# Kernel optimization log

Measured on AMD Instinct MI355X. Metric: run time of the kernel, lower is better.

Reference implementation:

```python
import jax, jax.numpy as jnp
import numpy as np

H = 16  # num_heads


def _sinusoidal_positions(n_pos, d, dtype=jnp.float32):
    half = d // 2
    freqs = 1.0 / 10000 ** (jnp.arange(0, half, dtype=dtype) / float(half))
    pos = jnp.arange(n_pos, dtype=dtype)[:, None]
    angles = pos * freqs[None, :]
    emb = jnp.concatenate([jnp.sin(angles), jnp.cos(angles)], axis=-1)
    if d % 2 == 1:
        emb = jnp.pad(emb, ((0, 0), (0, 1)))
    return emb.astype(dtype)


def setup_inputs() -> dict:
    key = jax.random.key(0)
    B, M, C = 64, 2048, 1024
    D = C // H
    ks = jax.random.split(key, 12)
    s = 1.0 / np.sqrt(C)
    return {
        "x": jax.random.normal(ks[0], (B, C), jnp.float32),
        "mem": jax.random.normal(ks[1], (B, M, C), jnp.float32),
        "Wq": jax.random.normal(ks[2], (C, C), jnp.float32) * s,
        "bq": jnp.zeros((C,), jnp.float32),
        "Wk": jax.random.normal(ks[3], (C, C), jnp.float32) * s,
        "bk": jnp.zeros((C,), jnp.float32),
        "Wv": jax.random.normal(ks[4], (C, C), jnp.float32) * s,
        "bv": jnp.zeros((C,), jnp.float32),
        "u_bias": jax.random.normal(ks[5], (H, D), jnp.float32) * 0.02,
        "v_bias": jax.random.normal(ks[6], (H, D), jnp.float32) * 0.02,
        "Wo": jax.random.normal(ks[7], (C, C), jnp.float32) * s,
        "bo": jnp.zeros((C,), jnp.float32),
    }


def reference(x, mem, Wq, bq, Wk, bk, Wv, bv, u_bias, v_bias, Wo, bo):
    B, C = x.shape
    D = C // H
    M = mem.shape[1]
    L = M + 1
    cat = jnp.concatenate([mem, x[:, None, :]], axis=1)  # (B, L, C)
    q = (x @ Wq + bq).reshape(B, H, D)
    k = (cat @ Wk + bk).reshape(B, L, H, D)
    v = (cat @ Wv + bv).reshape(B, L, H, D)
    r = _sinusoidal_positions(L, D)[::-1, :]  # (L, D), reversed
    scale = 1.0 / jnp.sqrt(jnp.float32(D))
    ac = jnp.einsum('bhd,blhd->bhl', q + u_bias[None, :, :], k)
    bd = jnp.einsum('bhd,ld->bhl', q + v_bias[None, :, :], r)
    attn = jax.nn.softmax((ac + bd) * scale, axis=-1)
    out = jnp.einsum('bhl,blhd->bhd', attn, v).reshape(B, C)
    return out @ Wo + bo
```

## Files before the change

### kernel.cpp

```cpp
#include <hip/hip_runtime.h>
#include <hip/hip_bf16.h>
#include <math.h>

#define B   64
#define C   1024
#define HH  16
#define DD  64
#define MM  2048
#define LL  2049
#define SCALE 0.125f
#define NCHC 9
#define CHC  228
#define LCH  16
#define LCHR 129

template <int CTRL>
__device__ __forceinline__ float dpp_add(float keep, float send) {
  int moved =
      __builtin_amdgcn_update_dpp(0, __float_as_int(send), CTRL, 0xF, 0xF, true);
  return keep + __int_as_float(moved);
}

__global__ __launch_bounds__(256) void k_gemm(
    const float* __restrict__ A, int a_row_stride, int a_bx_off,
    const float* __restrict__ W, float* __restrict__ P) {
  __shared__ __attribute__((aligned(16))) float a_s[64 * 132];
  __shared__ __attribute__((aligned(16))) float b_s[128 * 68];
  int t = threadIdx.x;
  int jt = blockIdx.x, kc = blockIdx.y;
  const float* Ab = A + (size_t)jt * a_bx_off;
  int k0 = kc * 128;
  for (int idx = t; idx < 2048; idx += 256) {
    int bb = idx >> 5, f4 = idx & 31;
    float4 v = *(const float4*)&Ab[(size_t)bb * a_row_stride + k0 + 4 * f4];
    *(float4*)&a_s[bb * 132 + 4 * f4] = v;
  }
  for (int idx = t; idx < 2048; idx += 256) {
    int kk = idx >> 4, f4 = idx & 15;
    float4 v = *(const float4*)&W[(size_t)(k0 + kk) * 1024 + jt * 64 + 4 * f4];
    *(float4*)&b_s[kk * 68 + 4 * f4] = v;
  }
  __syncthreads();
  int j0 = (t & 15) * 4, b0 = (t >> 4) * 4;
  float4 acc[4];
#pragma unroll
  for (int i = 0; i < 4; ++i) acc[i] = make_float4(0.f, 0.f, 0.f, 0.f);
  for (int k = 0; k < 128; k += 4) {
    float4 w0 = *(const float4*)&b_s[(k + 0) * 68 + j0];
    float4 w1 = *(const float4*)&b_s[(k + 1) * 68 + j0];
    float4 w2 = *(const float4*)&b_s[(k + 2) * 68 + j0];
    float4 w3 = *(const float4*)&b_s[(k + 3) * 68 + j0];
#pragma unroll
    for (int i = 0; i < 4; ++i) {
      float4 av = *(const float4*)&a_s[(b0 + i) * 132 + k];
      acc[i].x += av.x * w0.x + av.y * w1.x + av.z * w2.x + av.w * w3.x;
      acc[i].y += av.x * w0.y + av.y * w1.y + av.z * w2.y + av.w * w3.y;
      acc[i].z += av.x * w0.z + av.y * w1.z + av.z * w2.z + av.w * w3.z;
      acc[i].w += av.x * w0.w + av.y * w1.w + av.z * w2.w + av.w * w3.w;
    }
  }
  size_t ob = (size_t)kc * 65536 + jt * 64;
#pragma unroll
  for (int i = 0; i < 4; ++i)
    *(float4*)&P[ob + (size_t)(b0 + i) * 1024 + j0] = acc[i];
}

__global__ __launch_bounds__(256) void k_reduce_qp(
    const float* __restrict__ P, const float* __restrict__ bq,
    const float* __restrict__ u, const float* __restrict__ v,
    float* __restrict__ qu, float* __restrict__ qv) {
  int idx = blockIdx.x * 256 + threadIdx.x;
  int b = idx >> 8, f4 = idx & 255;
  size_t off = (size_t)b * 1024 + 4 * f4;
  float4 s = *(const float4*)&P[off];
#pragma unroll
  for (int kc = 1; kc < 8; ++kc) {
    float4 t4 = *(const float4*)&P[(size_t)kc * 65536 + off];
    s.x += t4.x; s.y += t4.y; s.z += t4.z; s.w += t4.w;
  }
  float4 bb = *(const float4*)&bq[4 * f4];
  s.x += bb.x; s.y += bb.y; s.z += bb.z; s.w += bb.w;
  float4 uu = *(const float4*)&u[4 * f4];
  float4 vv = *(const float4*)&v[4 * f4];
  float4 o1 = make_float4(s.x + uu.x, s.y + uu.y, s.z + uu.z, s.w + uu.w);
  float4 o2 = make_float4(s.x + vv.x, s.y + vv.y, s.z + vv.z, s.w + vv.w);
  *(float4*)&qu[off] = o1;
  *(float4*)&qv[off] = o2;
}

__global__ __launch_bounds__(256) void k_reduce1(
    const float* __restrict__ P, const float* __restrict__ bias,
    float* __restrict__ out) {
  int idx = blockIdx.x * 256 + threadIdx.x;
  int b = idx >> 8, f4 = idx & 255;
  size_t off = (size_t)b * 1024 + 4 * f4;
  float4 s = *(const float4*)&P[off];
#pragma unroll
  for (int kc = 1; kc < 8; ++kc) {
    float4 t4 = *(const float4*)&P[(size_t)kc * 65536 + off];
    s.x += t4.x; s.y += t4.y; s.z += t4.z; s.w += t4.w;
  }
  float4 bb = *(const float4*)&bias[4 * f4];
  s.x += bb.x; s.y += bb.y; s.z += bb.z; s.w += bb.w;
  *(float4*)&out[off] = s;
}

__global__ __launch_bounds__(256) void k_wtilde(
    const float* __restrict__ qu, const float* __restrict__ Wk,
    float* __restrict__ wt) {
  __shared__ __attribute__((aligned(16))) float a_s[64 * 68];
  __shared__ __attribute__((aligned(16))) float w_s[64 * 68];
  int t = threadIdx.x, ct = blockIdx.x, h = blockIdx.y;
  for (int idx = t; idx < 1024; idx += 256) {
    int bb = idx >> 4, f4 = idx & 15;
    *(float4*)&a_s[bb * 68 + 4 * f4] =
        *(const float4*)&qu[(size_t)bb * 1024 + h * 64 + 4 * f4];
  }
  for (int idx = t; idx < 1024; idx += 256) {
    int cc = idx >> 4, f4 = idx & 15;
    *(float4*)&w_s[cc * 68 + 4 * f4] =
        *(const float4*)&Wk[(size_t)(ct * 64 + cc) * 1024 + h * 64 + 4 * f4];
  }
  __syncthreads();
  int c0 = (t & 15) * 4, b0 = (t >> 4) * 4;
  float acc[4][4] = {};
  for (int d = 0; d < 64; d += 4) {
    float4 w0 = *(const float4*)&w_s[(c0 + 0) * 68 + d];
    float4 w1 = *(const float4*)&w_s[(c0 + 1) * 68 + d];
    float4 w2 = *(const float4*)&w_s[(c0 + 2) * 68 + d];
    float4 w3 = *(const float4*)&w_s[(c0 + 3) * 68 + d];
#pragma unroll
    for (int i = 0; i < 4; ++i) {
      float4 av = *(const float4*)&a_s[(b0 + i) * 68 + d];
      acc[i][0] += av.x * w0.x + av.y * w0.y + av.z * w0.z + av.w * w0.w;
      acc[i][1] += av.x * w1.x + av.y * w1.y + av.z * w1.z + av.w * w1.w;
      acc[i][2] += av.x * w2.x + av.y * w2.y + av.z * w2.z + av.w * w2.w;
      acc[i][3] += av.x * w3.x + av.y * w3.y + av.z * w3.z + av.w * w3.w;
    }
  }
#pragma unroll
  for (int i = 0; i < 4; ++i) {
    float4 o = make_float4(acc[i][0], acc[i][1], acc[i][2], acc[i][3]);
    *(float4*)&wt[(size_t)((b0 + i) * 16 + h) * 1024 + ct * 64 + c0] = o;
  }
}

__global__ void k_rtab(float* __restrict__ rtab) {
  int idx = blockIdx.x * 256 + threadIdx.x;
  if (idx >= LL * 64) return;
  int l = idx >> 6, d = idx & 63;
  float p = (float)(LL - 1 - l);
  int dd = d & 31;
  float f = 1.0f / powf(10000.0f, (float)dd * (1.0f / 32.0f));
  float a = p * f;
  rtab[idx] = (d < 32) ? sinf(a) : cosf(a);
}

__global__ __launch_bounds__(256) void k_bd(
    const float* __restrict__ qv, const float* __restrict__ rtab,
    float* __restrict__ bd) {
  __shared__ __attribute__((aligned(16))) float rt_s[128 * 68];
  int t = threadIdx.x, ch = blockIdx.x, b = blockIdx.y;
  int l0 = ch * 128;
  int nrows = min(128, LL - l0);
  for (int idx = t; idx < nrows * 16; idx += 256) {
    int r = idx >> 4, d4 = idx & 15;
    *(float4*)&rt_s[r * 68 + 4 * d4] =
        *(const float4*)&rtab[(size_t)(l0 + r) * 64 + 4 * d4];
  }
  __syncthreads();
  for (int idx = t; idx < 16 * 128; idx += 256) {
    int h = idx >> 7, r = idx & 127;
    if (r < nrows) {
      const float* qh = &qv[(size_t)b * 1024 + h * 64];
      const float* rr = &rt_s[r * 68];
      float s = 0.f;
#pragma unroll
      for (int d4 = 0; d4 < 16; ++d4) {
        float4 rv = *(const float4*)&rr[4 * d4];
        float4 qq = *(const float4*)&qh[4 * d4];
        s += rv.x * qq.x + rv.y * qq.y + rv.z * qq.z + rv.w * qq.w;
      }
      bd[(size_t)(b * 16 + h) * LL + l0 + r] = s;
    }
  }
}

__global__ __launch_bounds__(256, 4) void k_logits(
    const float* __restrict__ x, const float* __restrict__ mem,
    const float* __restrict__ wt, const float* __restrict__ bd,
    float* __restrict__ logits) {
  __shared__ float red_s[LCHR * 68];
  int t = threadIdx.x;
  int lane = t & 63, w = t >> 6;
  int b = blockIdx.y, ch = blockIdx.x;
  int l0 = ch * LCHR, lend = min(LL, l0 + LCHR);
  int c_off = w * 256 + lane * 4;
  float4 wr[16];
#pragma unroll
  for (int h = 0; h < 16; ++h)
    wr[h] = *(const float4*)&wt[(size_t)(b * 16 + h) * 1024 + c_off];
  const float* xrow = &x[(size_t)b * 1024 + c_off];
  const float* memb = &mem[(size_t)b * MM * 1024 + c_off];
  bool u0 = (lane & 1) != 0, u1 = (lane & 2) != 0;
  bool u2 = (lane & 4) != 0, u3 = (lane & 8) != 0;
  int hmap = ((lane & 1) << 3) | ((lane & 2) << 1) | ((lane & 4) >> 1) |
             ((lane & 8) >> 3);

#define LOADROWS(dst, base)                                                  \
  {                                                                          \
    _Pragma("unroll") for (int r = 0; r < 4; ++r) {                          \
      int l = min((base) + r, LL - 1);                                       \
      dst[r] = *(const float4*)((l < MM) ? &memb[(size_t)l * 1024] : xrow);  \
    }                                                                        \
  }
#define COMPROWS(src, base)                                                  \
  {                                                                          \
    _Pragma("unroll") for (int r = 0; r < 4; ++r) {                          \
      int row = (base) + r;                                                  \
      if (row < lend) {                                                      \
        float4 rv = src[r];                                                  \
        float p[16];                                                         \
        _Pragma("unroll") for (int h = 0; h < 16; ++h)                       \
            p[h] = rv.x * wr[h].x + rv.y * wr[h].y + rv.z * wr[h].z +        \
                   rv.w * wr[h].w;                                           \
        _Pragma("unroll") for (int i = 0; i < 8; ++i) {                      \
          float send = u0 ? p[i] : p[i + 8];                                 \
          float keep = u0 ? p[i + 8] : p[i];                                 \
          p[i] = dpp_add<0xB1>(keep, send);                                  \
        }                                                                    \
        _Pragma("unroll") for (int i = 0; i < 4; ++i) {                      \
          float send = u1 ? p[i] : p[i + 4];                                 \
          float keep = u1 ? p[i + 4] : p[i];                                 \
          p[i] = dpp_add<0x4E>(keep, send);                                  \
        }                                                                    \
        _Pragma("unroll") for (int i = 0; i < 2; ++i) {                      \
          float send = u2 ? p[i] : p[i + 2];                                 \
          float keep = u2 ? p[i + 2] : p[i];                                 \
          p[i] = keep + __shfl_xor(send, 4, 64);                             \
        }                                                                    \
        {                                                                    \
          float send = u3 ? p[0] : p[1];                                     \
          float keep = u3 ? p[1] : p[0];                                     \
          float u = dpp_add<0x128>(keep, send);                              \
          u += __shfl_xor(u, 16, 64);                                        \
          u += __shfl_xor(u, 32, 64);                                        \
          if (lane < 16) red_s[(row - l0) * 68 + w * 16 + hmap] = u;         \
        }                                                                    \
      }                                                                      \
    }                                                                        \
  }

  float4 rbA[4], rbB[4];
  LOADROWS(rbA, l0)
  for (int g0 = l0; g0 < lend; g0 += 8) {
    LOADROWS(rbB, g0 + 4)
    COMPROWS(rbA, g0)
    if (g0 + 8 < lend) LOADROWS(rbA, g0 + 8)
    COMPROWS(rbB, g0 + 4)
  }
#undef LOADROWS
#undef COMPROWS

  __syncthreads();
  int nrows = lend - l0;
  for (int idx = t; idx < 16 * LCHR; idx += 256) {
    int h = idx / LCHR, r = idx - h * LCHR;
    if (r < nrows) {
      float s = red_s[r * 68 + h] + red_s[r * 68 + 16 + h] +
                red_s[r * 68 + 32 + h] + red_s[r * 68 + 48 + h];
      int l = l0 + r;
      size_t o = (size_t)(b * 16 + h) * LL + l;
      logits[o] = (s + bd[o]) * SCALE;
    }
  }
}

__global__ __launch_bounds__(256) void k_softmax(float* __restrict__ logits) {
  __shared__ float red[8];
  int t = threadIdx.x;
  size_t base = (size_t)blockIdx.x * LL;
  float rv[9];
  float m = -1e30f;
#pragma unroll
  for (int k = 0; k < 9; ++k) {
    int i = t + k * 256;
    rv[k] = (i < LL) ? logits[base + i] : -1e30f;
    m = fmaxf(m, rv[k]);
  }
#pragma unroll
  for (int s = 1; s < 64; s <<= 1) m = fmaxf(m, __shfl_xor(m, s, 64));
  if ((t & 63) == 0) red[t >> 6] = m;
  __syncthreads();
  m = fmaxf(fmaxf(red[0], red[1]), fmaxf(red[2], red[3]));
  float sum = 0.f;
#pragma unroll
  for (int k = 0; k < 9; ++k) {
    int i = t + k * 256;
    float e = __expf(rv[k] - m);
    rv[k] = e;
    if (i < LL) sum += e;
  }
#pragma unroll
  for (int s = 1; s < 64; s <<= 1) sum += __shfl_xor(sum, s, 64);
  if ((t & 63) == 0) red[4 + (t >> 6)] = sum;
  __syncthreads();
  float inv = 1.0f / (red[4] + red[5] + red[6] + red[7]);
#pragma unroll
  for (int k = 0; k < 9; ++k) {
    int i = t + k * 256;
    if (i < LL) logits[base + i] = rv[k] * inv;
  }
}

__global__ __launch_bounds__(256) void k_ctx(
    const float* __restrict__ x, const float* __restrict__ mem,
    const float* __restrict__ attn, float* __restrict__ part) {
  __shared__ __attribute__((aligned(16))) float att_s[CHC * 20];
  int t = threadIdx.x;
  int lane = t & 63, w = t >> 6;
  int b = blockIdx.y;
  int ch = blockIdx.x >> 2, cq = blockIdx.x & 3;
  int l0 = ch * CHC, lend = min(LL, l0 + CHC);
  int natt = lend - l0;
  int c_off = cq * 256 + lane * 4;
#pragma unroll
  for (int h = 0; h < 16; ++h)
    for (int r = t; r < natt; r += 256)
      att_s[r * 20 + h] = attn[(size_t)(b * 16 + h) * LL + l0 + r];
  __syncthreads();
  float4 acc[16];
#pragma unroll
  for (int i = 0; i < 16; ++i) acc[i] = make_float4(0.f, 0.f, 0.f, 0.f);
  const float* xrow = &x[(size_t)b * 1024 + c_off];
  const float* memb = &mem[(size_t)b * MM * 1024 + c_off];

  for (int g0 = l0 + w * 8; g0 < lend; g0 += 32) {
    int nr = min(8, lend - g0);
    float4 rb[8];
#pragma unroll
    for (int r = 0; r < 8; ++r) {
      int l = g0 + r;
      rb[r] = *(const float4*)((l < MM) ? &memb[(size_t)l * 1024] : xrow);
    }
#pragma unroll
    for (int r = 0; r < 8; ++r) {
      if (r < nr) {
        int ri = g0 + r - l0;
        const float4* a4 = (const float4*)&att_s[ri * 20];
        float4 aA = a4[0], aB = a4[1], aC = a4[2], aD = a4[3];
        float4 rv = rb[r];
#define ACC1(i, s)                                                       \
  acc[i].x += (s) * rv.x; acc[i].y += (s) * rv.y;                        \
  acc[i].z += (s) * rv.z; acc[i].w += (s) * rv.w;
        ACC1(0, aA.x) ACC1(1, aA.y) ACC1(2, aA.z) ACC1(3, aA.w)
        ACC1(4, aB.x) ACC1(5, aB.y) ACC1(6, aB.z) ACC1(7, aB.w)
        ACC1(8, aC.x) ACC1(9, aC.y) ACC1(10, aC.z) ACC1(11, aC.w)
        ACC1(12, aD.x) ACC1(13, aD.y) ACC1(14, aD.z) ACC1(15, aD.w)
#undef ACC1
      }
    }
  }
  __syncthreads();
  float* accb = att_s;
  for (int ww = 0; ww < 4; ++ww) {
    if (w == ww) {
      if (ww == 0) {
#pragma unroll
        for (int h = 0; h < 16; ++h)
          *(float4*)&accb[h * 256 + lane * 4] = acc[h];
      } else {
#pragma unroll
        for (int h = 0; h < 16; ++h) {
          float4 vv = *(const float4*)&accb[h * 256 + lane * 4];
          vv.x += acc[h].x; vv.y += acc[h].y;
          vv.z += acc[h].z; vv.w += acc[h].w;
          *(float4*)&accb[h * 256 + lane * 4] = vv;
        }
      }
    }
    __syncthreads();
  }
  size_t pb = (size_t)((b * NCHC + ch) * 16) * 1024 + cq * 256;
  for (int idx = t; idx < 1024; idx += 256) {
    int h = idx >> 6, c4 = idx & 63;
    *(float4*)&part[pb + (size_t)h * 1024 + 4 * c4] =
        *(const float4*)&accb[h * 256 + 4 * c4];
  }
}

__global__ __launch_bounds__(256) void k_ctxreduce(
    const float* __restrict__ part, float* __restrict__ ctx) {
  int o4 = blockIdx.x * 256 + threadIdx.x;
  size_t o = (size_t)o4 * 4;
  int b = (int)(o >> 14);
  int rem = (int)(o & 16383);
  const float* p = &part[(size_t)b * (NCHC * 16384) + rem];
  float4 s = *(const float4*)p;
#pragma unroll
  for (int chk = 1; chk < NCHC; ++chk) {
    float4 v = *(const float4*)&p[(size_t)chk * 16384];
    s.x += v.x; s.y += v.y; s.z += v.z; s.w += v.w;
  }
  *(float4*)&ctx[o] = s;
}

extern "C" void kernel_launch(void* const* d_in, const int* in_sizes, int n_in,
                              void* d_out, int out_size, void* d_ws,
                              size_t ws_size, hipStream_t stream) {
  const float* x = (const float*)d_in[0];
  const float* mem = (const float*)d_in[1];
  const float* Wq = (const float*)d_in[2];
  const float* bq = (const float*)d_in[3];
  const float* Wk = (const float*)d_in[4];
  const float* Wv = (const float*)d_in[6];
  const float* bv = (const float*)d_in[7];
  const float* u_bias = (const float*)d_in[8];
  const float* v_bias = (const float*)d_in[9];
  const float* Wo = (const float*)d_in[10];
  const float* bo = (const float*)d_in[11];
  float* out = (float*)d_out;

  float* ws = (float*)d_ws;
  float* qu = ws;
  float* qv = qu + 65536;
  float* wt = qv + 65536;
  float* rtab = wt + 1048576;
  float* bd = rtab + 131200;
  float* logits = bd + 2098176;
  float* P = logits + 2098176;
  float* ctx = P + 524288;
  float* out1 = ctx + 1048576;
  float* part = out1 + 65536;

  k_gemm<<<dim3(16, 8), 256, 0, stream>>>(x, 1024, 0, Wq, P);
  k_rtab<<<dim3(513), 256, 0, stream>>>(rtab);
  k_reduce_qp<<<dim3(64), 256, 0, stream>>>(P, bq, u_bias, v_bias, qu, qv);
  k_wtilde<<<dim3(16, 16), 256, 0, stream>>>(qu, Wk, wt);
  k_bd<<<dim3(17, 64), 256, 0, stream>>>(qv, rtab, bd);
  k_logits<<<dim3(LCH, 64), 256, 0, stream>>>(x, mem, wt, bd, logits);
  k_softmax<<<dim3(1024), 256, 0, stream>>>(logits);
  k_ctx<<<dim3(36, 64), 256, 0, stream>>>(x, mem, logits, part);
  k_ctxreduce<<<dim3(1024), 256, 0, stream>>>(part, ctx);
  k_gemm<<<dim3(16, 8), 256, 0, stream>>>(ctx, 16384, 1024, Wv, P);
  k_reduce1<<<dim3(64), 256, 0, stream>>>(P, bv, out1);
  k_gemm<<<dim3(16, 8), 256, 0, stream>>>(out1, 1024, 0, Wo, P);
  k_reduce1<<<dim3(64), 256, 0, stream>>>(P, bo, out);
}
```

Measured before the change: 359.8 us.

## Fuse softmax into logits/ctx kernels and fold ctx chunk reduction into Wv GEMM

The logits kernel now emits per-chunk row max and exp-sum statistics, and the ctx kernel merges them to normalize the logits on the fly. This removes the standalone softmax pass over the attention matrix. The ctx partial-sum reduction kernel is also dropped: a new GEMM variant sums the 9 chunk partials while loading its A tile. Together these remove two kernel launches and a full read and write of logits and ctx, at the cost of some redundant exp and partial-sum work inside the remaining kernels.

```diff
diff --git a/kernel.cpp b/kernel.cpp
--- a/kernel.cpp
+++ b/kernel.cpp
@@ -65,6 +65,56 @@
     *(float4*)&P[ob + (size_t)(b0 + i) * 1024 + j0] = acc[i];
 }
 
+__global__ __launch_bounds__(256) void k_gemm_acc(
+    const float* __restrict__ part, const float* __restrict__ W,
+    float* __restrict__ P) {
+  __shared__ __attribute__((aligned(16))) float a_s[64 * 132];
+  __shared__ __attribute__((aligned(16))) float b_s[128 * 68];
+  int t = threadIdx.x;
+  int jt = blockIdx.x, kc = blockIdx.y;
+  int k0 = kc * 128;
+  for (int idx = t; idx < 2048; idx += 256) {
+    int bb = idx >> 5, f4 = idx & 31;
+    const float* pb =
+        &part[((size_t)(bb * NCHC) * 16 + jt) * 1024 + k0 + 4 * f4];
+    float4 v = *(const float4*)pb;
+#pragma unroll
+    for (int chk = 1; chk < NCHC; ++chk) {
+      float4 u = *(const float4*)&pb[(size_t)chk * 16384];
+      v.x += u.x; v.y += u.y; v.z += u.z; v.w += u.w;
+    }
+    *(float4*)&a_s[bb * 132 + 4 * f4] = v;
+  }
+  for (int idx = t; idx < 2048; idx += 256) {
+    int kk = idx >> 4, f4 = idx & 15;
+    float4 v = *(const float4*)&W[(size_t)(k0 + kk) * 1024 + jt * 64 + 4 * f4];
+    *(float4*)&b_s[kk * 68 + 4 * f4] = v;
+  }
+  __syncthreads();
+  int j0 = (t & 15) * 4, b0 = (t >> 4) * 4;
+  float4 acc[4];
+#pragma unroll
+  for (int i = 0; i < 4; ++i) acc[i] = make_float4(0.f, 0.f, 0.f, 0.f);
+  for (int k = 0; k < 128; k += 4) {
+    float4 w0 = *(const float4*)&b_s[(k + 0) * 68 + j0];
+    float4 w1 = *(const float4*)&b_s[(k + 1) * 68 + j0];
+    float4 w2 = *(const float4*)&b_s[(k + 2) * 68 + j0];
+    float4 w3 = *(const float4*)&b_s[(k + 3) * 68 + j0];
+#pragma unroll
+    for (int i = 0; i < 4; ++i) {
+      float4 av = *(const float4*)&a_s[(b0 + i) * 132 + k];
+      acc[i].x += av.x * w0.x + av.y * w1.x + av.z * w2.x + av.w * w3.x;
+      acc[i].y += av.x * w0.y + av.y * w1.y + av.z * w2.y + av.w * w3.y;
+      acc[i].z += av.x * w0.z + av.y * w1.z + av.z * w2.z + av.w * w3.z;
+      acc[i].w += av.x * w0.w + av.y * w1.w + av.z * w2.w + av.w * w3.w;
+    }
+  }
+  size_t ob = (size_t)kc * 65536 + jt * 64;
+#pragma unroll
+  for (int i = 0; i < 4; ++i)
+    *(float4*)&P[ob + (size_t)(b0 + i) * 1024 + j0] = acc[i];
+}
+
 __global__ __launch_bounds__(256) void k_reduce_qp(
     const float* __restrict__ P, const float* __restrict__ bq,
     const float* __restrict__ u, const float* __restrict__ v,
@@ -189,7 +239,7 @@
 __global__ __launch_bounds__(256, 4) void k_logits(
     const float* __restrict__ x, const float* __restrict__ mem,
     const float* __restrict__ wt, const float* __restrict__ bd,
-    float* __restrict__ logits) {
+    float* __restrict__ logits, float* __restrict__ ms) {
   __shared__ float red_s[LCHR * 68];
   int t = threadIdx.x;
   int lane = t & 63, w = t >> 6;
@@ -264,59 +314,47 @@
 
   __syncthreads();
   int nrows = lend - l0;
-  for (int idx = t; idx < 16 * LCHR; idx += 256) {
-    int h = idx / LCHR, r = idx - h * LCHR;
+  int h = t >> 4, sub = t & 15;
+  float lov[9];
+  float m = -3e38f;
+#pragma unroll
+  for (int i = 0; i < 9; ++i) {
+    int r = sub + 16 * i;
+    float lo = -3e38f;
     if (r < nrows) {
-      float s = red_s[r * 68 + h] + red_s[r * 68 + 16 + h] +
-                red_s[r * 68 + 32 + h] + red_s[r * 68 + 48 + h];
-      int l = l0 + r;
-      size_t o = (size_t)(b * 16 + h) * LL + l;
-      logits[o] = (s + bd[o]) * SCALE;
-    }
-  }
-}
-
-__global__ __launch_bounds__(256) void k_softmax(float* __restrict__ logits) {
-  __shared__ float red[8];
-  int t = threadIdx.x;
-  size_t base = (size_t)blockIdx.x * LL;
-  float rv[9];
-  float m = -1e30f;
-#pragma unroll
-  for (int k = 0; k < 9; ++k) {
-    int i = t + k * 256;
-    rv[k] = (i < LL) ? logits[base + i] : -1e30f;
-    m = fmaxf(m, rv[k]);
-  }
-#pragma unroll
-  for (int s = 1; s < 64; s <<= 1) m = fmaxf(m, __shfl_xor(m, s, 64));
-  if ((t & 63) == 0) red[t >> 6] = m;
-  __syncthreads();
-  m = fmaxf(fmaxf(red[0], red[1]), fmaxf(red[2], red[3]));
-  float sum = 0.f;
-#pragma unroll
-  for (int k = 0; k < 9; ++k) {
-    int i = t + k * 256;
-    float e = __expf(rv[k] - m);
-    rv[k] = e;
-    if (i < LL) sum += e;
-  }
-#pragma unroll
-  for (int s = 1; s < 64; s <<= 1) sum += __shfl_xor(sum, s, 64);
-  if ((t & 63) == 0) red[4 + (t >> 6)] = sum;
-  __syncthreads();
-  float inv = 1.0f / (red[4] + red[5] + red[6] + red[7]);
-#pragma unroll
-  for (int k = 0; k < 9; ++k) {
-    int i = t + k * 256;
-    if (i < LL) logits[base + i] = rv[k] * inv;
+      float s4 = red_s[r * 68 + h] + red_s[r * 68 + 16 + h] +
+                 red_s[r * 68 + 32 + h] + red_s[r * 68 + 48 + h];
+      size_t o = (size_t)(b * 16 + h) * LL + l0 + r;
+      lo = (s4 + bd[o]) * SCALE;
+      logits[o] = lo;
+    }
+    lov[i] = lo;
+    m = fmaxf(m, lo);
+  }
+  m = fmaxf(m, __shfl_xor(m, 1, 64));
+  m = fmaxf(m, __shfl_xor(m, 2, 64));
+  m = fmaxf(m, __shfl_xor(m, 4, 64));
+  m = fmaxf(m, __shfl_xor(m, 8, 64));
+  float ssum = 0.f;
+#pragma unroll
+  for (int i = 0; i < 9; ++i) ssum += __expf(lov[i] - m);
+  ssum += __shfl_xor(ssum, 1, 64);
+  ssum += __shfl_xor(ssum, 2, 64);
+  ssum += __shfl_xor(ssum, 4, 64);
+  ssum += __shfl_xor(ssum, 8, 64);
+  if (sub == 0) {
+    size_t mo = ((size_t)b * LCH + ch) * 32 + h * 2;
+    ms[mo] = m;
+    ms[mo + 1] = ssum;
   }
 }
 
 __global__ __launch_bounds__(256) void k_ctx(
     const float* __restrict__ x, const float* __restrict__ mem,
-    const float* __restrict__ attn, float* __restrict__ part) {
+    const float* __restrict__ logits, const float* __restrict__ ms,
+    float* __restrict__ part) {
   __shared__ __attribute__((aligned(16))) float att_s[CHC * 20];
+  __shared__ float m_l[16], inv_l[16];
   int t = threadIdx.x;
   int lane = t & 63, w = t >> 6;
   int b = blockIdx.y;
@@ -324,10 +362,26 @@
   int l0 = ch * CHC, lend = min(LL, l0 + CHC);
   int natt = lend - l0;
   int c_off = cq * 256 + lane * 4;
+  if (t < 16) {
+    float M = -3e38f;
+#pragma unroll
+    for (int cc = 0; cc < LCH; ++cc)
+      M = fmaxf(M, ms[((size_t)b * LCH + cc) * 32 + t * 2]);
+    float den = 0.f;
+#pragma unroll
+    for (int cc = 0; cc < LCH; ++cc)
+      den += __expf(ms[((size_t)b * LCH + cc) * 32 + t * 2] - M) *
+             ms[((size_t)b * LCH + cc) * 32 + t * 2 + 1];
+    m_l[t] = M;
+    inv_l[t] = 1.0f / den;
+  }
+  __syncthreads();
 #pragma unroll
   for (int h = 0; h < 16; ++h)
-    for (int r = t; r < natt; r += 256)
-      att_s[r * 20 + h] = attn[(size_t)(b * 16 + h) * LL + l0 + r];
+    for (int r = t; r < natt; r += 256) {
+      float lo = logits[(size_t)(b * 16 + h) * LL + l0 + r];
+      att_s[r * 20 + h] = __expf(lo - m_l[h]) * inv_l[h];
+    }
   __syncthreads();
   float4 acc[16];
 #pragma unroll
@@ -389,22 +443,6 @@
   }
 }
 
-__global__ __launch_bounds__(256) void k_ctxreduce(
-    const float* __restrict__ part, float* __restrict__ ctx) {
-  int o4 = blockIdx.x * 256 + threadIdx.x;
-  size_t o = (size_t)o4 * 4;
-  int b = (int)(o >> 14);
-  int rem = (int)(o & 16383);
-  const float* p = &part[(size_t)b * (NCHC * 16384) + rem];
-  float4 s = *(const float4*)p;
-#pragma unroll
-  for (int chk = 1; chk < NCHC; ++chk) {
-    float4 v = *(const float4*)&p[(size_t)chk * 16384];
-    s.x += v.x; s.y += v.y; s.z += v.z; s.w += v.w;
-  }
-  *(float4*)&ctx[o] = s;
-}
-
 extern "C" void kernel_launch(void* const* d_in, const int* in_sizes, int n_in,
                               void* d_out, int out_size, void* d_ws,
                               size_t ws_size, hipStream_t stream) {
@@ -428,9 +466,9 @@
   float* rtab = wt + 1048576;
   float* bd = rtab + 131200;
   float* logits = bd + 2098176;
-  float* P = logits + 2098176;
-  float* ctx = P + 524288;
-  float* out1 = ctx + 1048576;
+  float* ms = logits + 2098176;
+  float* P = ms + 32768;
+  float* out1 = P + 524288;
   float* part = out1 + 65536;
 
   k_gemm<<<dim3(16, 8), 256, 0, stream>>>(x, 1024, 0, Wq, P);
@@ -438,11 +476,9 @@
   k_reduce_qp<<<dim3(64), 256, 0, stream>>>(P, bq, u_bias, v_bias, qu, qv);
   k_wtilde<<<dim3(16, 16), 256, 0, stream>>>(qu, Wk, wt);
   k_bd<<<dim3(17, 64), 256, 0, stream>>>(qv, rtab, bd);
-  k_logits<<<dim3(LCH, 64), 256, 0, stream>>>(x, mem, wt, bd, logits);
-  k_softmax<<<dim3(1024), 256, 0, stream>>>(logits);
-  k_ctx<<<dim3(36, 64), 256, 0, stream>>>(x, mem, logits, part);
-  k_ctxreduce<<<dim3(1024), 256, 0, stream>>>(part, ctx);
-  k_gemm<<<dim3(16, 8), 256, 0, stream>>>(ctx, 16384, 1024, Wv, P);
+  k_logits<<<dim3(LCH, 64), 256, 0, stream>>>(x, mem, wt, bd, logits, ms);
+  k_ctx<<<dim3(36, 64), 256, 0, stream>>>(x, mem, logits, ms, part);
+  k_gemm_acc<<<dim3(16, 8), 256, 0, stream>>>(part, Wv, P);
   k_reduce1<<<dim3(64), 256, 0, stream>>>(P, bv, out1);
   k_gemm<<<dim3(16, 8), 256, 0, stream>>>(out1, 1024, 0, Wo, P);
   k_reduce1<<<dim3(64), 256, 0, stream>>>(P, bo, out);
```

Measured after the change: 354.9 us. No clear change (-1.3%).
